# Kernel tuning notes

Measured on AMD Instinct MI355X. Metric: run time of the kernel, lower is better.

The kernel has to match this reference:

```python
import math
import jax, jax.numpy as jnp
import numpy as np

B, S, H, DQ, DV = 2, 2048, 16, 192, 128
NEG_INF = jnp.float32(-1e30)


def setup_inputs() -> dict:
    key = jax.random.key(0)
    kq, kk, kv = jax.random.split(key, 3)
    q = jax.random.normal(kq, (B, S, H, DQ), dtype=jnp.float32)
    k = jax.random.normal(kk, (B, S, H, DQ), dtype=jnp.float32)
    v = jax.random.normal(kv, (B, S, H, DV), dtype=jnp.float32)
    return {"q": q, "k": k, "v": v}


def reference(q, k, v):
    # Causal MLA attention, BSHD layout, asymmetric QK vs V head dims.
    dq = q.shape[-1]
    scale = jnp.asarray(math.sqrt(1.0 / dq), dtype=q.dtype)  # default 1/sqrt(dq)
    # scores: [B, H, S, S]
    scores = jnp.einsum("bqhd,bkhd->bhqk", q, k) * scale
    s = q.shape[1]
    causal = jnp.tril(jnp.ones((s, s), dtype=bool))  # qidx >= kidx
    scores = jnp.where(causal[None, None, :, :], scores, NEG_INF)
    p = jax.nn.softmax(scores, axis=-1)
    # out: [B, S, H, DV]
    out = jnp.einsum("bhqk,bkhd->bqhd", p, v)
    return out
```

## Files before the change

kernel.cpp:

```cpp
#include <hip/hip_runtime.h>

#define B_ 2
#define S_ 2048
#define H_ 16
#define DQ_ 192
#define DV_ 128
#define SCL2 0.10411163731422901f

typedef short short8 __attribute__((ext_vector_type(8)));
typedef float f32x4 __attribute__((ext_vector_type(4)));
typedef float f32x16 __attribute__((ext_vector_type(16)));
typedef unsigned uint2v __attribute__((ext_vector_type(2)));

#define KG_BYTES ((size_t)25165824)
#define VG_BYTES ((size_t)16777216)

__device__ __forceinline__ unsigned short f2bf(float f) {
  union { float f; unsigned u; } x; x.f = f;
  unsigned r = x.u + 0x7FFFu + ((x.u >> 16) & 1u);
  return (unsigned short)(r >> 16);
}

__device__ __forceinline__ float hw_exp2(float x) {
  float r; asm("v_exp_f32 %0, %1" : "=v"(r) : "v"(x)); return r;
}
__device__ __forceinline__ unsigned cvtpk(float lo, float hi) {
  unsigned r; asm("v_cvt_pk_bf16_f32 %0, %1, %2" : "=v"(r) : "v"(lo), "v"(hi)); return r;
}
__device__ __forceinline__ float max3f(float a, float b, float c) {
  float r; asm("v_max3_f32 %0, %1, %2, %3" : "=v"(r) : "v"(a), "v"(b), "v"(c)); return r;
}
__device__ __forceinline__ float pl32max(float x) {
  uint2v r = __builtin_amdgcn_permlane32_swap(__float_as_uint(x), __float_as_uint(x), false, false);
  return fmaxf(__uint_as_float(r[0]), __uint_as_float(r[1]));
}
__device__ __forceinline__ float pl32add(float x) {
  uint2v r = __builtin_amdgcn_permlane32_swap(__float_as_uint(x), __float_as_uint(x), false, false);
  return __uint_as_float(r[0]) + __uint_as_float(r[1]);
}

#define GLL16(src, dst) \
  __builtin_amdgcn_global_load_lds((const __attribute__((address_space(1))) void*)(src), \
                                   (__attribute__((address_space(3))) void*)(dst), 16, 0, 0)

__global__ __launch_bounds__(256) void prep_kv(const float* __restrict__ K,
                                               const float* __restrict__ V,
                                               unsigned short* __restrict__ Kg,
                                               unsigned short* __restrict__ Vg) {
  __shared__ float lv[64][132];
  const int bid = blockIdx.x;
  const int tid = threadIdx.x;
  if (bid < 12288) {
    int idx = bid * 256 + tid;
    int d4 = idx % 48; int r = idx / 48;
    int h = r % H_; r /= H_;
    int s = r % S_; int b = r / S_;
    float4 f = *(const float4*)(K + (size_t)((b * S_ + s) * H_ + h) * DQ_ + d4 * 4);
    ushort4 u; u.x = f2bf(f.x); u.y = f2bf(f.y); u.z = f2bf(f.z); u.w = f2bf(f.w);
    size_t rowb = (size_t)((b * H_ + h) * S_ + s) * (DQ_ * 2);
    int cb = (d4 * 8) ^ ((s & 7) << 4);
    *(ushort4*)((char*)Kg + rowb + cb) = u;
  } else {
    int blk = bid - 12288;
    int tile = blk & 31, bh = blk >> 5;
    int b = bh >> 4, h = bh & 15;
    #pragma unroll
    for (int it = 0; it < 8; ++it) {
      int idx = it * 256 + tid;
      int s_in = idx >> 5, d4 = idx & 31;
      float4 f = *(const float4*)(V + (size_t)((b * S_ + tile * 64 + s_in) * H_ + h) * DV_ + d4 * 4);
      lv[s_in][d4 * 4 + 0] = f.x; lv[s_in][d4 * 4 + 1] = f.y;
      lv[s_in][d4 * 4 + 2] = f.z; lv[s_in][d4 * 4 + 3] = f.w;
    }
    __syncthreads();
    char* base = (char*)Vg + (size_t)blk * 16384;
    #pragma unroll
    for (int it = 0; it < 4; ++it) {
      int ch = it * 256 + tid;
      int pr = ch >> 4, ci = ch & 15;
      int orig = ci ^ (pr & 15);
      int dv = pr * 2 + (orig >> 3);
      int k0 = (orig & 7) * 8;
      short8 u;
      #pragma unroll
      for (int e = 0; e < 8; ++e) u[e] = (short)f2bf(lv[k0 + e][dv]);
      *(short8*)(base + ch * 16) = u;
    }
  }
}

__launch_bounds__(512, 1)
__global__ void mla_fwd(const float* __restrict__ Q,
                        const unsigned short* __restrict__ Kg,
                        const unsigned short* __restrict__ Vg,
                        float* __restrict__ O) {
  __shared__ __align__(16) unsigned char SB[3][40960];

  const int tid  = threadIdx.x;
  const int wid  = tid >> 6;
  const int lane = tid & 63;
  const int l31  = lane & 31;
  const int hi   = lane >> 5;
  const int hi16 = hi * 16;
  const int qg   = wid & 3;
  const int kh   = wid >> 2;

  const int i  = blockIdx.x;
  const int x  = i & 7;
  const int li = i >> 3;
  const int bh = x * 4 + (li >> 3);
  const int jj = li & 7;
  const int b  = bh >> 4, h = bh & 15;

  const char* kg_bh = (const char*)Kg + (size_t)bh * S_ * (DQ_ * 2);
  const char* vg_bh = (const char*)Vg + (size_t)bh * 32 * 16384;

  const int kxor = (lane & 7) << 4;
  const int prl  = l31 >> 1;
  const int nb_  = (lane & 1) * 8 + hi;
  int voff[2];
  #pragma unroll
  for (int ks = 0; ks < 2; ++ks) {
    int n = nb_ + kh * 4 + ks * 2;
    voff[ks] = prl * 256 + ((n ^ prl) << 4);
  }

  #define STAGE(buf)                                                              \
    do {                                                                          \
      _Pragma("unroll")                                                           \
      for (int ci = 0; ci < 5; ++ci) {                                            \
        const int cc = wid * 5 + ci;                                              \
        const char* src = (cc < 24) ? (kSp + ci * 1024) : (vSp + ci * 1024);      \
        GLL16(src, &SB[buf][cc * 1024]);                                          \
      }                                                                           \
      kSp += 24576; vSp += 16384;                                                 \
    } while (0)

  for (int job = 0; job < 2; ++job) {
    const int qt  = job ? jj : (15 - jj);
    const int wq0 = qt * 128 + qg * 32;
    const int qln = wq0 + l31;

    short8 qf[12];
    {
      const size_t qoff = (size_t)((b * S_ + qln) * H_ + h) * DQ_;
      #pragma unroll
      for (int d0 = 0; d0 < 12; ++d0) {
        const float* p = Q + qoff + d0 * 16 + hi * 8;
        float4 f0 = *(const float4*)(p);
        float4 f1 = *(const float4*)(p + 4);
        short8 a;
        a[0] = f2bf(f0.x * SCL2); a[1] = f2bf(f0.y * SCL2);
        a[2] = f2bf(f0.z * SCL2); a[3] = f2bf(f0.w * SCL2);
        a[4] = f2bf(f1.x * SCL2); a[5] = f2bf(f1.y * SCL2);
        a[6] = f2bf(f1.z * SCL2); a[7] = f2bf(f1.w * SCL2);
        qf[d0] = a;
      }
    }

    f32x16 o4[4];
    #pragma unroll
    for (int t2 = 0; t2 < 4; ++t2) o4[t2] = (f32x16)0.0f;
    float m = -1e30f, l = 0.0f;

    const int ntiles = 2 * qt + 2;

    const char* kSp = kg_bh + wid * 5120 + lane * 16;
    const char* vSp = vg_bh - 24576 + wid * 5120 + lane * 16;

    STAGE(0);
    if (ntiles > 1) STAGE(1);

    int bc = 0;
    for (int kt = 0; kt < ntiles; ++kt) {
      if (kt + 1 < ntiles) asm volatile("s_waitcnt vmcnt(5)" ::: "memory");
      else                 asm volatile("s_waitcnt vmcnt(0)" ::: "memory");
      __builtin_amdgcn_s_barrier();
      if (kt + 2 < ntiles) {
        int bs = bc - 1; if (bs < 0) bs = 2;
        STAGE(bs);
      }

      const int kbase = kt * 64;
      const int khb = kbase + kh * 32;

      if (khb <= wq0 + 31) {
        const char* kr = (const char*)&SB[bc][0] + (kh * 32 + l31) * 384;
        f32x16 s = (f32x16)0.0f;
        __builtin_amdgcn_s_setprio(1);
        #pragma unroll
        for (int d0 = 0; d0 < 12; ++d0) {
          const int col = (d0 * 32 + hi16) ^ kxor;
          s = __builtin_amdgcn_mfma_f32_32x32x16_bf16(*(const short8*)(kr + col), qf[d0], s, 0, 0, 0);
        }
        __builtin_amdgcn_s_setprio(0);

        const char* vb = (const char*)&SB[bc][0] + 24576;
        short8 v00 = *(const short8*)(vb + 0 * 4096 + voff[0]);
        short8 v01 = *(const short8*)(vb + 0 * 4096 + voff[1]);
        short8 v10 = *(const short8*)(vb + 1 * 4096 + voff[0]);
        short8 v11 = *(const short8*)(vb + 1 * 4096 + voff[1]);
        short8 v20 = *(const short8*)(vb + 2 * 4096 + voff[0]);
        short8 v21 = *(const short8*)(vb + 2 * 4096 + voff[1]);
        short8 v30 = *(const short8*)(vb + 3 * 4096 + voff[0]);
        short8 v31 = *(const short8*)(vb + 3 * 4096 + voff[1]);

        float p_[16];
        #pragma unroll
        for (int r = 0; r < 16; ++r) p_[r] = s[r];
        if (khb + 31 > wq0) {
          const int rem = qln - khb - 4 * hi;
          #pragma unroll
          for (int r = 0; r < 16; ++r) {
            const int kof = (r & 3) + 8 * (r >> 2);
            if (kof > rem) p_[r] = -1e30f;
          }
        }

        float mA = max3f(max3f(p_[0], p_[1], p_[2]),
                         max3f(p_[3], p_[4], p_[5]),
                         max3f(p_[6], p_[7], p_[8]));
        float mB = max3f(max3f(p_[9], p_[10], p_[11]),
                         max3f(p_[12], p_[13], p_[14]),
                         p_[15]);
        float mx = pl32max(fmaxf(mA, mB));
        if (__any(mx > m + 8.0f)) {
          float mn = fmaxf(m, mx);
          float al = hw_exp2(m - mn);
          #pragma unroll
          for (int t2 = 0; t2 < 4; ++t2) o4[t2] *= al;
          l *= al; m = mn;
        }
        #pragma unroll
        for (int rr = 0; rr < 16; ++rr) p_[rr] = hw_exp2(p_[rr] - m);
        float a8[8];
        #pragma unroll
        for (int r = 0; r < 8; ++r) a8[r] = p_[r] + p_[8 + r];
        float a4[4];
        #pragma unroll
        for (int r = 0; r < 4; ++r) a4[r] = a8[r] + a8[4 + r];
        l += (a4[0] + a4[1]) + (a4[2] + a4[3]);

        unsigned a_ = cvtpk(p_[0], p_[1]),   b2_ = cvtpk(p_[2], p_[3]);
        unsigned c_ = cvtpk(p_[4], p_[5]),   d_  = cvtpk(p_[6], p_[7]);
        unsigned e_ = cvtpk(p_[8], p_[9]),   f_  = cvtpk(p_[10], p_[11]);
        unsigned g_ = cvtpk(p_[12], p_[13]), h_  = cvtpk(p_[14], p_[15]);
        uint2v s02 = __builtin_amdgcn_permlane32_swap(a_, c_, false, false);
        uint2v s13 = __builtin_amdgcn_permlane32_swap(b2_, d_, false, false);
        uint2v s46 = __builtin_amdgcn_permlane32_swap(e_, g_, false, false);
        uint2v s57 = __builtin_amdgcn_permlane32_swap(f_, h_, false, false);
        union { unsigned u[4]; short8 s; } pb0, pb1;
        pb0.u[0] = s02[0]; pb0.u[1] = s13[0]; pb0.u[2] = s02[1]; pb0.u[3] = s13[1];
        pb1.u[0] = s46[0]; pb1.u[1] = s57[0]; pb1.u[2] = s46[1]; pb1.u[3] = s57[1];

        __builtin_amdgcn_s_setprio(1);
        o4[0] = __builtin_amdgcn_mfma_f32_32x32x16_bf16(v00, pb0.s, o4[0], 0, 0, 0);
        o4[0] = __builtin_amdgcn_mfma_f32_32x32x16_bf16(v01, pb1.s, o4[0], 0, 0, 0);
        o4[1] = __builtin_amdgcn_mfma_f32_32x32x16_bf16(v10, pb0.s, o4[1], 0, 0, 0);
        o4[1] = __builtin_amdgcn_mfma_f32_32x32x16_bf16(v11, pb1.s, o4[1], 0, 0, 0);
        o4[2] = __builtin_amdgcn_mfma_f32_32x32x16_bf16(v20, pb0.s, o4[2], 0, 0, 0);
        o4[2] = __builtin_amdgcn_mfma_f32_32x32x16_bf16(v21, pb1.s, o4[2], 0, 0, 0);
        o4[3] = __builtin_amdgcn_mfma_f32_32x32x16_bf16(v30, pb0.s, o4[3], 0, 0, 0);
        o4[3] = __builtin_amdgcn_mfma_f32_32x32x16_bf16(v31, pb1.s, o4[3], 0, 0, 0);
        __builtin_amdgcn_s_setprio(0);
      }

      ++bc; if (bc == 3) bc = 0;
    }

    float lr = pl32add(l);
    __syncthreads();
    char* mrg = (char*)&SB[0][0];
    if (kh == 1) {
      float* po = (float*)(mrg + qg * 17408 + lane * 272);
      #pragma unroll
      for (int t2 = 0; t2 < 4; ++t2) {
        #pragma unroll
        for (int rr = 0; rr < 4; ++rr) {
          float4 st = { o4[t2][rr * 4 + 0], o4[t2][rr * 4 + 1],
                        o4[t2][rr * 4 + 2], o4[t2][rr * 4 + 3] };
          *(float4*)(po + t2 * 16 + rr * 4) = st;
        }
      }
      float* pm = (float*)(mrg + 69632 + (qg * 64 + lane) * 8);
      pm[0] = m; pm[1] = lr;
    }
    __syncthreads();
    if (kh == 0) {
      const float* po = (const float*)(mrg + qg * 17408 + lane * 272);
      const float* pm = (const float*)(mrg + 69632 + (qg * 64 + lane) * 8);
      const float mB = pm[0], lB = pm[1];
      const float ms = fmaxf(m, mB);
      const float wA = hw_exp2(m - ms), wB = hw_exp2(mB - ms);
      const float inv = 1.0f / (lr * wA + lB * wB);
      float* ob = O + (size_t)((b * S_ + qln) * H_ + h) * DV_;
      #pragma unroll
      for (int t2 = 0; t2 < 4; ++t2) {
        #pragma unroll
        for (int rr = 0; rr < 4; ++rr) {
          float4 vb4 = *(const float4*)(po + t2 * 16 + rr * 4);
          float4 st = { (o4[t2][rr * 4 + 0] * wA + vb4.x * wB) * inv,
                        (o4[t2][rr * 4 + 1] * wA + vb4.y * wB) * inv,
                        (o4[t2][rr * 4 + 2] * wA + vb4.z * wB) * inv,
                        (o4[t2][rr * 4 + 3] * wA + vb4.w * wB) * inv };
          *(float4*)(ob + t2 * 32 + rr * 8 + hi * 4) = st;
        }
      }
    }
    __syncthreads();
  }
  #undef STAGE
}

__launch_bounds__(256)
__global__ void mla_fwd_fb(const float* __restrict__ Q,
                           const float* __restrict__ K,
                           const float* __restrict__ V,
                           float* __restrict__ O) {
  __shared__ __align__(16) unsigned short Kl[2][32][200];
  __shared__ __align__(16) unsigned short Vt[2][128][40];
  __shared__ __align__(16) unsigned short Pl[4][16][40];
  const int tid = threadIdx.x, wid = tid >> 6, lane = tid & 63;
  const int l15 = lane & 15, g = lane >> 4;
  const int qtile = (int)gridDim.x - 1 - (int)blockIdx.x;
  const int bh = blockIdx.y, b = bh >> 4, h = bh & 15;
  const int q0w = qtile * 64 + wid * 16;
  const int krs = H_ * DQ_, vrs = H_ * DV_;
  short8 aq[6];
  {
    const int qoff = ((b * S_ + (q0w + l15)) * H_ + h) * DQ_;
    #pragma unroll
    for (int d0 = 0; d0 < 6; ++d0) {
      const float* p = Q + qoff + d0 * 32 + g * 8;
      float4 f0 = *(const float4*)(p); float4 f1 = *(const float4*)(p + 4);
      short8 a;
      a[0]=f2bf(f0.x); a[1]=f2bf(f0.y); a[2]=f2bf(f0.z); a[3]=f2bf(f0.w);
      a[4]=f2bf(f1.x); a[5]=f2bf(f1.y); a[6]=f2bf(f1.z); a[7]=f2bf(f1.w);
      aq[d0] = a;
    }
  }
  f32x4 o[8];
  #pragma unroll
  for (int t = 0; t < 8; ++t) o[t] = (f32x4)0.0f;
  float m[4], l[4];
  #pragma unroll
  for (int r = 0; r < 4; ++r) { m[r] = -1e30f; l[r] = 0.0f; }
  const int ntiles = qtile * 2 + 2;
  float4 kr[6], vr[4];
  {
    const float* Kb = K + ((b * S_) * H_ + h) * DQ_;
    #pragma unroll
    for (int i = 0; i < 6; ++i) { int idx = i*256+tid; int row = idx/48, c4 = idx%48;
      kr[i] = *(const float4*)(Kb + row*krs + c4*4); }
    const float* Vb = V + ((b * S_) * H_ + h) * DV_;
    #pragma unroll
    for (int i = 0; i < 4; ++i) { int idx = i*256+tid; int row = idx&31, c4 = idx>>5;
      vr[i] = *(const float4*)(Vb + row*vrs + c4*4); }
    #pragma unroll
    for (int i = 0; i < 6; ++i) { int idx = i*256+tid; int row = idx/48, c4 = idx%48;
      ushort4 u; u.x=f2bf(kr[i].x); u.y=f2bf(kr[i].y); u.z=f2bf(kr[i].z); u.w=f2bf(kr[i].w);
      *(ushort4*)&Kl[0][row][c4*4] = u; }
    #pragma unroll
    for (int i = 0; i < 4; ++i) { int idx = i*256+tid; int row = idx&31, c4 = idx>>5;
      Vt[0][c4*4+0][row]=f2bf(vr[i].x); Vt[0][c4*4+1][row]=f2bf(vr[i].y);
      Vt[0][c4*4+2][row]=f2bf(vr[i].z); Vt[0][c4*4+3][row]=f2bf(vr[i].w); }
  }
  __syncthreads();
  int cur = 0;
  for (int kt = 0; kt < ntiles; ++kt) {
    const int kbase = kt * 32;
    const bool pf = (kt + 1 < ntiles);
    if (pf) {
      const int nb = kbase + 32;
      const float* Kb = K + ((b*S_+nb)*H_ + h)*DQ_;
      #pragma unroll
      for (int i = 0; i < 6; ++i) { int idx = i*256+tid; int row = idx/48, c4 = idx%48;
        kr[i] = *(const float4*)(Kb + row*krs + c4*4); }
      const float* Vb = V + ((b*S_+nb)*H_ + h)*DV_;
      #pragma unroll
      for (int i = 0; i < 4; ++i) { int idx = i*256+tid; int row = idx&31, c4 = idx>>5;
        vr[i] = *(const float4*)(Vb + row*vrs + c4*4); }
    }
    f32x4 sa0 = (f32x4)0.0f, sa1 = (f32x4)0.0f;
    #pragma unroll
    for (int d0 = 0; d0 < 6; ++d0) {
      short8 b0 = *(const short8*)&Kl[cur][l15][d0*32 + g*8];
      sa0 = __builtin_amdgcn_mfma_f32_16x16x32_bf16(aq[d0], b0, sa0, 0, 0, 0);
      short8 b1 = *(const short8*)&Kl[cur][16+l15][d0*32 + g*8];
      sa1 = __builtin_amdgcn_mfma_f32_16x16x32_bf16(aq[d0], b1, sa1, 0, 0, 0);
    }
    float p0[4], p1[4];
    #pragma unroll
    for (int r = 0; r < 4; ++r) {
      const int qg = q0w + 4*g + r;
      float s0 = sa0[r]*SCL2, s1 = sa1[r]*SCL2;
      if (kbase + l15 > qg) s0 = -1e30f;
      if (kbase + 16 + l15 > qg) s1 = -1e30f;
      p0[r] = s0; p1[r] = s1;
    }
    #pragma unroll
    for (int r = 0; r < 4; ++r) {
      float rm = fmaxf(p0[r], p1[r]);
      #pragma unroll
      for (int off = 1; off < 16; off <<= 1) rm = fmaxf(rm, __shfl_xor(rm, off));
      float mn = fmaxf(m[r], rm);
      float alpha = exp2f(m[r] - mn); m[r] = mn;
      float e0 = exp2f(p0[r] - mn), e1 = exp2f(p1[r] - mn);
      p0[r] = e0; p1[r] = e1;
      float rsum = e0 + e1;
      #pragma unroll
      for (int off = 1; off < 16; off <<= 1) rsum += __shfl_xor(rsum, off);
      l[r] = l[r]*alpha + rsum;
      #pragma unroll
      for (int t = 0; t < 8; ++t) o[t][r] *= alpha;
    }
    #pragma unroll
    for (int r = 0; r < 4; ++r) {
      Pl[wid][4*g+r][l15]      = f2bf(p0[r]);
      Pl[wid][4*g+r][16+l15]   = f2bf(p1[r]);
    }
    short8 pa = *(const short8*)&Pl[wid][l15][g*8];
    #pragma unroll
    for (int t = 0; t < 8; ++t) {
      short8 vb = *(const short8*)&Vt[cur][t*16+l15][g*8];
      o[t] = __builtin_amdgcn_mfma_f32_16x16x32_bf16(pa, vb, o[t], 0, 0, 0);
    }
    if (pf) {
      #pragma unroll
      for (int i = 0; i < 6; ++i) { int idx = i*256+tid; int row = idx/48, c4 = idx%48;
        ushort4 u; u.x=f2bf(kr[i].x); u.y=f2bf(kr[i].y); u.z=f2bf(kr[i].z); u.w=f2bf(kr[i].w);
        *(ushort4*)&Kl[cur^1][row][c4*4] = u; }
      #pragma unroll
      for (int i = 0; i < 4; ++i) { int idx = i*256+tid; int row = idx&31, c4 = idx>>5;
        Vt[cur^1][c4*4+0][row]=f2bf(vr[i].x); Vt[cur^1][c4*4+1][row]=f2bf(vr[i].y);
        Vt[cur^1][c4*4+2][row]=f2bf(vr[i].z); Vt[cur^1][c4*4+3][row]=f2bf(vr[i].w); }
    }
    __syncthreads();
    cur ^= 1;
  }
  #pragma unroll
  for (int r = 0; r < 4; ++r) {
    const int qg = q0w + 4*g + r;
    const float inv = 1.0f / l[r];
    #pragma unroll
    for (int t = 0; t < 8; ++t)
      O[((b*S_+qg)*H_ + h)*DV_ + t*16 + l15] = o[t][r] * inv;
  }
}

extern "C" void kernel_launch(void* const* d_in, const int* in_sizes, int n_in,
                              void* d_out, int out_size, void* d_ws, size_t ws_size,
                              hipStream_t stream) {
  const float* q = (const float*)d_in[0];
  const float* k = (const float*)d_in[1];
  const float* v = (const float*)d_in[2];
  float* out = (float*)d_out;

  if (ws_size >= KG_BYTES + VG_BYTES) {
    unsigned short* Kg = (unsigned short*)d_ws;
    unsigned short* Vg = (unsigned short*)((char*)d_ws + KG_BYTES);
    prep_kv<<<dim3(12288 + B_ * H_ * 32), dim3(256), 0, stream>>>(k, v, Kg, Vg);
    mla_fwd<<<dim3(256), dim3(512), 0, stream>>>(q, Kg, Vg, out);
  } else {
    dim3 grid(S_ / 64, B_ * H_);
    mla_fwd_fb<<<grid, dim3(256), 0, stream>>>(q, k, v, out);
  }
}
```

Measured before the change: 90.56 us.

## Halve block waves and have each wave process two 32-row query subtiles

The attention kernel now launches 256 threads (4 waves) instead of 512. Each wave holds two 32-row query fragments and reuses every K fragment loaded from LDS for two QK MFMAs, then runs the softmax/PV step once per subtile. Staging work per wave doubles (10 global-to-LDS loads per tile), and the cross-wave merge handles two subtiles per wave. This cuts LDS reads of K and the per-block wave count, at the cost of higher register pressure (two Q fragment sets, two output accumulators) and less latency hiding from fewer waves.

```diff
diff --git a/kernel.cpp b/kernel.cpp
--- a/kernel.cpp
+++ b/kernel.cpp
@@ -89,7 +89,7 @@
   }
 }
 
-__launch_bounds__(512, 1)
+__launch_bounds__(256, 1)
 __global__ void mla_fwd(const float* __restrict__ Q,
                         const unsigned short* __restrict__ Kg,
                         const unsigned short* __restrict__ Vg,
@@ -102,8 +102,8 @@
   const int l31  = lane & 31;
   const int hi   = lane >> 5;
   const int hi16 = hi * 16;
-  const int qg   = wid & 3;
-  const int kh   = wid >> 2;
+  const int qg   = wid & 1;
+  const int kh   = wid >> 1;
 
   const int i  = blockIdx.x;
   const int x  = i & 7;
@@ -128,21 +128,77 @@
   #define STAGE(buf)                                                              \
     do {                                                                          \
       _Pragma("unroll")                                                           \
-      for (int ci = 0; ci < 5; ++ci) {                                            \
-        const int cc = wid * 5 + ci;                                              \
+      for (int ci = 0; ci < 10; ++ci) {                                           \
+        const int cc = wid * 10 + ci;                                             \
         const char* src = (cc < 24) ? (kSp + ci * 1024) : (vSp + ci * 1024);      \
         GLL16(src, &SB[buf][cc * 1024]);                                          \
       }                                                                           \
       kSp += 24576; vSp += 16384;                                                 \
     } while (0)
 
+  #define PROC_SUB(SACC, QB, MS, LS, OS)                                          \
+    {                                                                             \
+      float p_[16];                                                               \
+      _Pragma("unroll") for (int r = 0; r < 16; ++r) p_[r] = SACC[r];             \
+      if (khb + 31 > (QB)) {                                                      \
+        const int rem = (QB) + l31 - khb - 4 * hi;                                \
+        _Pragma("unroll") for (int r = 0; r < 16; ++r) {                          \
+          const int kof = (r & 3) + 8 * (r >> 2);                                 \
+          if (kof > rem) p_[r] = -1e30f;                                          \
+        }                                                                         \
+      }                                                                           \
+      float tA = max3f(max3f(p_[0], p_[1], p_[2]),                                \
+                       max3f(p_[3], p_[4], p_[5]),                                \
+                       max3f(p_[6], p_[7], p_[8]));                               \
+      float tB = max3f(max3f(p_[9], p_[10], p_[11]),                              \
+                       max3f(p_[12], p_[13], p_[14]),                             \
+                       p_[15]);                                                   \
+      float mx = pl32max(fmaxf(tA, tB));                                          \
+      if (__any(mx > MS + 8.0f)) {                                                \
+        float mn = fmaxf(MS, mx);                                                 \
+        float al = hw_exp2(MS - mn);                                              \
+        _Pragma("unroll") for (int t2 = 0; t2 < 4; ++t2) OS[t2] *= al;            \
+        LS *= al; MS = mn;                                                        \
+      }                                                                           \
+      _Pragma("unroll") for (int rr = 0; rr < 16; ++rr) p_[rr] = hw_exp2(p_[rr] - MS); \
+      float a8[8];                                                                \
+      _Pragma("unroll") for (int r = 0; r < 8; ++r) a8[r] = p_[r] + p_[8 + r];    \
+      float a4[4];                                                                \
+      _Pragma("unroll") for (int r = 0; r < 4; ++r) a4[r] = a8[r] + a8[4 + r];    \
+      LS += (a4[0] + a4[1]) + (a4[2] + a4[3]);                                    \
+      unsigned a_ = cvtpk(p_[0], p_[1]),   b2_ = cvtpk(p_[2], p_[3]);             \
+      unsigned c_ = cvtpk(p_[4], p_[5]),   d_  = cvtpk(p_[6], p_[7]);             \
+      unsigned e_ = cvtpk(p_[8], p_[9]),   f_  = cvtpk(p_[10], p_[11]);           \
+      unsigned g_ = cvtpk(p_[12], p_[13]), h_  = cvtpk(p_[14], p_[15]);           \
+      uint2v s02 = __builtin_amdgcn_permlane32_swap(a_, c_, false, false);        \
+      uint2v s13 = __builtin_amdgcn_permlane32_swap(b2_, d_, false, false);       \
+      uint2v s46 = __builtin_amdgcn_permlane32_swap(e_, g_, false, false);        \
+      uint2v s57 = __builtin_amdgcn_permlane32_swap(f_, h_, false, false);        \
+      union { unsigned u[4]; short8 s; } pb0, pb1;                                \
+      pb0.u[0] = s02[0]; pb0.u[1] = s13[0]; pb0.u[2] = s02[1]; pb0.u[3] = s13[1]; \
+      pb1.u[0] = s46[0]; pb1.u[1] = s57[0]; pb1.u[2] = s46[1]; pb1.u[3] = s57[1]; \
+      __builtin_amdgcn_s_setprio(1);                                              \
+      OS[0] = __builtin_amdgcn_mfma_f32_32x32x16_bf16(v00, pb0.s, OS[0], 0, 0, 0);\
+      OS[0] = __builtin_amdgcn_mfma_f32_32x32x16_bf16(v01, pb1.s, OS[0], 0, 0, 0);\
+      OS[1] = __builtin_amdgcn_mfma_f32_32x32x16_bf16(v10, pb0.s, OS[1], 0, 0, 0);\
+      OS[1] = __builtin_amdgcn_mfma_f32_32x32x16_bf16(v11, pb1.s, OS[1], 0, 0, 0);\
+      OS[2] = __builtin_amdgcn_mfma_f32_32x32x16_bf16(v20, pb0.s, OS[2], 0, 0, 0);\
+      OS[2] = __builtin_amdgcn_mfma_f32_32x32x16_bf16(v21, pb1.s, OS[2], 0, 0, 0);\
+      OS[3] = __builtin_amdgcn_mfma_f32_32x32x16_bf16(v30, pb0.s, OS[3], 0, 0, 0);\
+      OS[3] = __builtin_amdgcn_mfma_f32_32x32x16_bf16(v31, pb1.s, OS[3], 0, 0, 0);\
+      __builtin_amdgcn_s_setprio(0);                                              \
+    }
+
   for (int job = 0; job < 2; ++job) {
     const int qt  = job ? jj : (15 - jj);
-    const int wq0 = qt * 128 + qg * 32;
-    const int qln = wq0 + l31;
-
-    short8 qf[12];
-    {
+    const int wq0 = qt * 128 + qg * 64;
+    const int qA  = wq0;
+    const int qB  = wq0 + 32;
+
+    short8 qfA[12], qfB[12];
+    #pragma unroll
+    for (int s = 0; s < 2; ++s) {
+      const int qln = (s ? qB : qA) + l31;
       const size_t qoff = (size_t)((b * S_ + qln) * H_ + h) * DQ_;
       #pragma unroll
       for (int d0 = 0; d0 < 12; ++d0) {
@@ -154,26 +210,26 @@
         a[2] = f2bf(f0.z * SCL2); a[3] = f2bf(f0.w * SCL2);
         a[4] = f2bf(f1.x * SCL2); a[5] = f2bf(f1.y * SCL2);
         a[6] = f2bf(f1.z * SCL2); a[7] = f2bf(f1.w * SCL2);
-        qf[d0] = a;
+        if (s) qfB[d0] = a; else qfA[d0] = a;
       }
     }
 
-    f32x16 o4[4];
-    #pragma unroll
-    for (int t2 = 0; t2 < 4; ++t2) o4[t2] = (f32x16)0.0f;
-    float m = -1e30f, l = 0.0f;
+    f32x16 oA[4], oB[4];
+    #pragma unroll
+    for (int t2 = 0; t2 < 4; ++t2) { oA[t2] = (f32x16)0.0f; oB[t2] = (f32x16)0.0f; }
+    float m0 = -1e30f, l0 = 0.0f, m1 = -1e30f, l1 = 0.0f;
 
     const int ntiles = 2 * qt + 2;
 
-    const char* kSp = kg_bh + wid * 5120 + lane * 16;
-    const char* vSp = vg_bh - 24576 + wid * 5120 + lane * 16;
+    const char* kSp = kg_bh + wid * 10240 + lane * 16;
+    const char* vSp = vg_bh - 24576 + wid * 10240 + lane * 16;
 
     STAGE(0);
     if (ntiles > 1) STAGE(1);
 
     int bc = 0;
     for (int kt = 0; kt < ntiles; ++kt) {
-      if (kt + 1 < ntiles) asm volatile("s_waitcnt vmcnt(5)" ::: "memory");
+      if (kt + 1 < ntiles) asm volatile("s_waitcnt vmcnt(10)" ::: "memory");
       else                 asm volatile("s_waitcnt vmcnt(0)" ::: "memory");
       __builtin_amdgcn_s_barrier();
       if (kt + 2 < ntiles) {
@@ -184,14 +240,16 @@
       const int kbase = kt * 64;
       const int khb = kbase + kh * 32;
 
-      if (khb <= wq0 + 31) {
+      if (khb <= wq0 + 63) {
         const char* kr = (const char*)&SB[bc][0] + (kh * 32 + l31) * 384;
-        f32x16 s = (f32x16)0.0f;
+        f32x16 sA = (f32x16)0.0f, sB = (f32x16)0.0f;
         __builtin_amdgcn_s_setprio(1);
         #pragma unroll
         for (int d0 = 0; d0 < 12; ++d0) {
           const int col = (d0 * 32 + hi16) ^ kxor;
-          s = __builtin_amdgcn_mfma_f32_32x32x16_bf16(*(const short8*)(kr + col), qf[d0], s, 0, 0, 0);
+          short8 kf = *(const short8*)(kr + col);
+          sA = __builtin_amdgcn_mfma_f32_32x32x16_bf16(kf, qfA[d0], sA, 0, 0, 0);
+          sB = __builtin_amdgcn_mfma_f32_32x32x16_bf16(kf, qfB[d0], sB, 0, 0, 0);
         }
         __builtin_amdgcn_s_setprio(0);
 
@@ -205,111 +263,73 @@
         short8 v30 = *(const short8*)(vb + 3 * 4096 + voff[0]);
         short8 v31 = *(const short8*)(vb + 3 * 4096 + voff[1]);
 
-        float p_[16];
-        #pragma unroll
-        for (int r = 0; r < 16; ++r) p_[r] = s[r];
-        if (khb + 31 > wq0) {
-          const int rem = qln - khb - 4 * hi;
-          #pragma unroll
-          for (int r = 0; r < 16; ++r) {
-            const int kof = (r & 3) + 8 * (r >> 2);
-            if (kof > rem) p_[r] = -1e30f;
-          }
+        PROC_SUB(sB, qB, m1, l1, oB)
+        if (khb <= qA + 31) {
+          PROC_SUB(sA, qA, m0, l0, oA)
         }
-
-        float mA = max3f(max3f(p_[0], p_[1], p_[2]),
-                         max3f(p_[3], p_[4], p_[5]),
-                         max3f(p_[6], p_[7], p_[8]));
-        float mB = max3f(max3f(p_[9], p_[10], p_[11]),
-                         max3f(p_[12], p_[13], p_[14]),
-                         p_[15]);
-        float mx = pl32max(fmaxf(mA, mB));
-        if (__any(mx > m + 8.0f)) {
-          float mn = fmaxf(m, mx);
-          float al = hw_exp2(m - mn);
-          #pragma unroll
-          for (int t2 = 0; t2 < 4; ++t2) o4[t2] *= al;
-          l *= al; m = mn;
-        }
-        #pragma unroll
-        for (int rr = 0; rr < 16; ++rr) p_[rr] = hw_exp2(p_[rr] - m);
-        float a8[8];
-        #pragma unroll
-        for (int r = 0; r < 8; ++r) a8[r] = p_[r] + p_[8 + r];
-        float a4[4];
-        #pragma unroll
-        for (int r = 0; r < 4; ++r) a4[r] = a8[r] + a8[4 + r];
-        l += (a4[0] + a4[1]) + (a4[2] + a4[3]);
-
-        unsigned a_ = cvtpk(p_[0], p_[1]),   b2_ = cvtpk(p_[2], p_[3]);
-        unsigned c_ = cvtpk(p_[4], p_[5]),   d_  = cvtpk(p_[6], p_[7]);
-        unsigned e_ = cvtpk(p_[8], p_[9]),   f_  = cvtpk(p_[10], p_[11]);
-        unsigned g_ = cvtpk(p_[12], p_[13]), h_  = cvtpk(p_[14], p_[15]);
-        uint2v s02 = __builtin_amdgcn_permlane32_swap(a_, c_, false, false);
-        uint2v s13 = __builtin_amdgcn_permlane32_swap(b2_, d_, false, false);
-        uint2v s46 = __builtin_amdgcn_permlane32_swap(e_, g_, false, false);
-        uint2v s57 = __builtin_amdgcn_permlane32_swap(f_, h_, false, false);
-        union { unsigned u[4]; short8 s; } pb0, pb1;
-        pb0.u[0] = s02[0]; pb0.u[1] = s13[0]; pb0.u[2] = s02[1]; pb0.u[3] = s13[1];
-        pb1.u[0] = s46[0]; pb1.u[1] = s57[0]; pb1.u[2] = s46[1]; pb1.u[3] = s57[1];
-
-        __builtin_amdgcn_s_setprio(1);
-        o4[0] = __builtin_amdgcn_mfma_f32_32x32x16_bf16(v00, pb0.s, o4[0], 0, 0, 0);
-        o4[0] = __builtin_amdgcn_mfma_f32_32x32x16_bf16(v01, pb1.s, o4[0], 0, 0, 0);
-        o4[1] = __builtin_amdgcn_mfma_f32_32x32x16_bf16(v10, pb0.s, o4[1], 0, 0, 0);
-        o4[1] = __builtin_amdgcn_mfma_f32_32x32x16_bf16(v11, pb1.s, o4[1], 0, 0, 0);
-        o4[2] = __builtin_amdgcn_mfma_f32_32x32x16_bf16(v20, pb0.s, o4[2], 0, 0, 0);
-        o4[2] = __builtin_amdgcn_mfma_f32_32x32x16_bf16(v21, pb1.s, o4[2], 0, 0, 0);
-        o4[3] = __builtin_amdgcn_mfma_f32_32x32x16_bf16(v30, pb0.s, o4[3], 0, 0, 0);
-        o4[3] = __builtin_amdgcn_mfma_f32_32x32x16_bf16(v31, pb1.s, o4[3], 0, 0, 0);
-        __builtin_amdgcn_s_setprio(0);
       }
 
       ++bc; if (bc == 3) bc = 0;
     }
 
-    float lr = pl32add(l);
+    float lr0 = pl32add(l0);
+    float lr1 = pl32add(l1);
     __syncthreads();
     char* mrg = (char*)&SB[0][0];
     if (kh == 1) {
-      float* po = (float*)(mrg + qg * 17408 + lane * 272);
-      #pragma unroll
-      for (int t2 = 0; t2 < 4; ++t2) {
+      #pragma unroll
+      for (int s = 0; s < 2; ++s) {
+        const int vq = qg * 2 + s;
+        float* po = (float*)(mrg + vq * 17408 + lane * 272);
         #pragma unroll
-        for (int rr = 0; rr < 4; ++rr) {
-          float4 st = { o4[t2][rr * 4 + 0], o4[t2][rr * 4 + 1],
-                        o4[t2][rr * 4 + 2], o4[t2][rr * 4 + 3] };
-          *(float4*)(po + t2 * 16 + rr * 4) = st;
+        for (int t2 = 0; t2 < 4; ++t2) {
+          #pragma unroll
+          for (int rr = 0; rr < 4; ++rr) {
+            f32x16* oS = s ? oB : oA;
+            float4 st = { oS[t2][rr * 4 + 0], oS[t2][rr * 4 + 1],
+                          oS[t2][rr * 4 + 2], oS[t2][rr * 4 + 3] };
+            *(float4*)(po + t2 * 16 + rr * 4) = st;
+          }
+        }
+        float* pm = (float*)(mrg + 69632 + (vq * 64 + lane) * 8);
+        pm[0] = s ? m1 : m0;
+        pm[1] = s ? lr1 : lr0;
+      }
+    }
+    __syncthreads();
+    if (kh == 0) {
+      #pragma unroll
+      for (int s = 0; s < 2; ++s) {
+        const int vq = qg * 2 + s;
+        const float* po = (const float*)(mrg + vq * 17408 + lane * 272);
+        const float* pm = (const float*)(mrg + 69632 + (vq * 64 + lane) * 8);
+        const float mO = s ? m1 : m0;
+        const float lO = s ? lr1 : lr0;
+        const float mX = pm[0], lX = pm[1];
+        const float ms = fmaxf(mO, mX);
+        const float wA = hw_exp2(mO - ms), wB = hw_exp2(mX - ms);
+        const float inv = 1.0f / (lO * wA + lX * wB);
+        const int qln = (s ? qB : qA) + l31;
+        float* ob = O + (size_t)((b * S_ + qln) * H_ + h) * DV_;
+        f32x16* oS = s ? oB : oA;
+        #pragma unroll
+        for (int t2 = 0; t2 < 4; ++t2) {
+          #pragma unroll
+          for (int rr = 0; rr < 4; ++rr) {
+            float4 vb4 = *(const float4*)(po + t2 * 16 + rr * 4);
+            float4 st = { (oS[t2][rr * 4 + 0] * wA + vb4.x * wB) * inv,
+                          (oS[t2][rr * 4 + 1] * wA + vb4.y * wB) * inv,
+                          (oS[t2][rr * 4 + 2] * wA + vb4.z * wB) * inv,
+                          (oS[t2][rr * 4 + 3] * wA + vb4.w * wB) * inv };
+            *(float4*)(ob + t2 * 32 + rr * 8 + hi * 4) = st;
+          }
         }
       }
-      float* pm = (float*)(mrg + 69632 + (qg * 64 + lane) * 8);
-      pm[0] = m; pm[1] = lr;
     }
     __syncthreads();
-    if (kh == 0) {
-      const float* po = (const float*)(mrg + qg * 17408 + lane * 272);
-      const float* pm = (const float*)(mrg + 69632 + (qg * 64 + lane) * 8);
-      const float mB = pm[0], lB = pm[1];
-      const float ms = fmaxf(m, mB);
-      const float wA = hw_exp2(m - ms), wB = hw_exp2(mB - ms);
-      const float inv = 1.0f / (lr * wA + lB * wB);
-      float* ob = O + (size_t)((b * S_ + qln) * H_ + h) * DV_;
-      #pragma unroll
-      for (int t2 = 0; t2 < 4; ++t2) {
-        #pragma unroll
-        for (int rr = 0; rr < 4; ++rr) {
-          float4 vb4 = *(const float4*)(po + t2 * 16 + rr * 4);
-          float4 st = { (o4[t2][rr * 4 + 0] * wA + vb4.x * wB) * inv,
-                        (o4[t2][rr * 4 + 1] * wA + vb4.y * wB) * inv,
-                        (o4[t2][rr * 4 + 2] * wA + vb4.z * wB) * inv,
-                        (o4[t2][rr * 4 + 3] * wA + vb4.w * wB) * inv };
-          *(float4*)(ob + t2 * 32 + rr * 8 + hi * 4) = st;
-        }
-      }
-    }
-    __syncthreads();
   }
   #undef STAGE
+  #undef PROC_SUB
 }
 
 __launch_bounds__(256)
@@ -460,7 +480,7 @@
     unsigned short* Kg = (unsigned short*)d_ws;
     unsigned short* Vg = (unsigned short*)((char*)d_ws + KG_BYTES);
     prep_kv<<<dim3(12288 + B_ * H_ * 32), dim3(256), 0, stream>>>(k, v, Kg, Vg);
-    mla_fwd<<<dim3(256), dim3(512), 0, stream>>>(q, Kg, Vg, out);
+    mla_fwd<<<dim3(256), dim3(256), 0, stream>>>(q, Kg, Vg, out);
   } else {
     dim3 grid(S_ / 64, B_ * H_);
     mla_fwd_fb<<<grid, dim3(256), 0, stream>>>(q, k, v, out);
```

Result: slower. 128.5 us (+41.9%).
